# Kernel tuning notes

Hardware: AMD Instinct MI355X
Metric: run time of the kernel (lower is better)

The kernel has to match this reference:

```python
import jax, jax.numpy as jnp
import numpy as np
from itertools import combinations

B, J, D, H, L, DFF = 2048, 7, 128, 8, 4, 512
TH, GH = 4, 4  # triplet cross-attn heads (min(4,128//32)), group-transformer heads

def _build_static():
    trips = list(combinations(range(J), 3))
    tid = {t: i for i, t in enumerate(trips)}
    member = np.zeros((J, len(trips)), dtype=bool)
    for i, t in enumerate(trips):
        for j in t:
            member[j, i] = True
    isr_l, g1_l, g2_l = [], [], []
    for isr in range(J):
        rem = [j for j in range(J) if j != isr]
        for c in combinations(rem, 3):
            comp = tuple(j for j in rem if j not in c)
            if c < comp:
                isr_l.append(isr); g1_l.append(c); g2_l.append(comp)
    return (np.array(trips), member, np.array(isr_l), np.array(g1_l), np.array(g2_l),
            np.array([tid[t] for t in g1_l]), np.array([tid[t] for t in g2_l]))

TRIPS, MEMBER, ISR_IDX, G1_JETS, G2_JETS, G1_TID, G2_TID = _build_static()
N_ASSIGN = len(ISR_IDX)  # 70
TCA_MASK = np.where(MEMBER, 0.0, -1e9).astype(np.float32)  # (J, 35) jet-restricted mask

def _gelu(x):
    return jax.nn.gelu(x, approximate=False)

def _ln(x, g, b, eps=1e-5):
    mu = x.mean(-1, keepdims=True)
    v = ((x - mu) ** 2).mean(-1, keepdims=True)
    return (x - mu) / jnp.sqrt(v + eps) * g + b

def _attend(q, k, v, nhead, bias=None):
    Bq, Lq, d = q.shape
    Lk = k.shape[1]
    dh = d // nhead
    qh = q.reshape(Bq, Lq, nhead, dh)
    kh = k.reshape(Bq, Lk, nhead, dh)
    vh = v.reshape(Bq, Lk, nhead, dh)
    s = jnp.einsum('bqhd,bkhd->bhqk', qh, kh) / np.float32(np.sqrt(dh))
    if bias is not None:
        s = s + bias
    a = jax.nn.softmax(s, -1)
    return jnp.einsum('bhqk,bkhd->bqhd', a, vh).reshape(Bq, Lq, d)

def _enc_layer(x, Wqkv, bqkv, Wo, bo, g1, b1, g2, b2, W1, bb1, W2, bb2, nhead, bias=None):
    # pre-LN TransformerEncoderLayer (norm_first=True, relu activation, eval mode)
    h = _ln(x, g1, b1)
    q, k, v = jnp.split(h @ Wqkv + bqkv, 3, axis=-1)
    x = x + _attend(q, k, v, nhead, bias) @ Wo + bo
    h2 = _ln(x, g2, b2)
    return x + jax.nn.relu(h2 @ W1 + bb1) @ W2 + bb2

def _feat6(p):
    E, px, py, pz = p[..., 0], p[..., 1], p[..., 2], p[..., 3]
    pt = jnp.sqrt(px ** 2 + py ** 2)
    p3 = jnp.sqrt(pt ** 2 + pz ** 2)
    m = jnp.sqrt(jnp.maximum(E ** 2 - p3 ** 2, 1e-8))
    eta = jnp.arcsinh(pz / jnp.maximum(pt, 1e-8))
    phi = jnp.arctan2(py, px)
    return jnp.stack([m, pt, eta, phi, E, p3], -1)

def _forward(four_momenta, W_in, b_in, pt_w, dr_w, mass_w, enc_Wqkv, enc_bqkv, enc_Wo, enc_bo, enc_g1, enc_b1, enc_g2, enc_b2, enc_W1, enc_bb1, enc_W2, enc_bb2, tca_Wq, tca_bq, tca_Wk, tca_bk, tca_Wv, tca_bv, tca_Wo, tca_bo, tca_g1, tca_b1, tca_W1, tca_bb1, tca_W2, tca_bb2, tca_g2, tca_b2, gt_Wqkv, gt_bqkv, gt_Wo, gt_bo, gt_g1, gt_b1, gt_g2, gt_b2, gt_W1, gt_bb1, gt_W2, gt_bb2, ph_g, ph_b, s_W1, s_b1, s_W2, s_b2, s_W3, s_b3):
    fm = four_momenta
    E, px, py, pz = fm[..., 0], fm[..., 1], fm[..., 2], fm[..., 3]
    pt = jnp.maximum(jnp.sqrt(px ** 2 + py ** 2), 1e-8)
    log_pt = jnp.log(pt)
    eta = jnp.arcsinh(pz / pt)
    phi = jnp.arctan2(py, px)
    m_jet = jnp.sqrt(jnp.maximum(E ** 2 - px ** 2 - py ** 2 - pz ** 2, 1e-8))
    x = jnp.concatenate([fm, jnp.stack([log_pt, eta, phi, m_jet], -1)], -1) @ W_in + b_in

    # fused per-head additive attention biases: pT hierarchy, deltaR, pair invariant mass
    pt_b = log_pt[:, :, None] - log_pt[:, None, :]
    cphi, sphi = px / pt, py / pt
    deta = eta[:, :, None] - eta[:, None, :]
    cdphi = jnp.clip(cphi[:, :, None] * cphi[:, None, :] + sphi[:, :, None] * sphi[:, None, :], -1.0 + 1e-7, 1.0 - 1e-7)
    dr_b = jnp.sqrt(deta ** 2 + jnp.arccos(cdphi) ** 2)
    Es = E[:, :, None] + E[:, None, :]
    ps2 = (px[:, :, None] + px[:, None, :]) ** 2 + (py[:, :, None] + py[:, None, :]) ** 2 + (pz[:, :, None] + pz[:, None, :]) ** 2
    mass_b = 0.5 * jnp.log(jnp.maximum(Es ** 2 - ps2, 1e-8))
    bias = (pt_w[None, :, None, None] * pt_b[:, None] + dr_w[None, :, None, None] * dr_b[:, None] + mass_w[None, :, None, None] * mass_b[:, None])  # (B,H,J,J)

    for i in range(L):
        x = _enc_layer(x, enc_Wqkv[i], enc_bqkv[i], enc_Wo[i], enc_bo[i], enc_g1[i], enc_b1[i], enc_g2[i], enc_b2[i], enc_W1[i], enc_bb1[i], enc_W2[i], enc_bb2[i], H, bias)
    jet_emb = x  # (B, J, D)

    # jet-restricted triplet cross-attention over the C(7,3)=35 triplet bank
    triplet_emb = jet_emb[:, TRIPS].mean(2)  # (B, 35, D)
    q = jet_emb @ tca_Wq + tca_bq
    k = triplet_emb @ tca_Wk + tca_bk
    v = triplet_emb @ tca_Wv + tca_bv
    attn = _attend(q, k, v, TH, jnp.asarray(TCA_MASK)[None, None]) @ tca_Wo + tca_bo
    jet_emb = _ln(jet_emb + attn, tca_g1, tca_b1)
    ff = _gelu(jet_emb @ tca_W1 + tca_bb1) @ tca_W2 + tca_bb2
    jet_emb = _ln(jet_emb + ff, tca_g2, tca_b2)

    # GroupTransformer over all unique 3-jet groups in parallel, mean-pool readout
    nT = len(TRIPS)
    gt_in = jet_emb[:, TRIPS].reshape(B * nT, 3, D)
    gt_out = _enc_layer(gt_in, gt_Wqkv, gt_bqkv, gt_Wo, gt_bo, gt_g1, gt_b1, gt_g2, gt_b2, gt_W1, gt_bb1, gt_W2, gt_bb2, GH)
    group_emb = gt_out.mean(1).reshape(B, nT, D)  # (B, 35, D)

    g1e = group_emb[:, G1_TID]  # (B, 70, D)
    g2e = group_emb[:, G2_TID]
    pair_sum = g1e + g2e
    pair_prod = g1e * g2e
    pair_sqdiff = (g1e - g2e) ** 2
    isr_emb = jet_emb[:, ISR_IDX]  # (B, 70, D)
    event_emb = jnp.broadcast_to(jet_emb.mean(1)[:, None], (B, N_ASSIGN, D))

    p_g1 = fm[:, G1_JETS].sum(2)  # (B, 70, 4)
    p_g2 = fm[:, G2_JETS].sum(2)
    p_isr = fm[:, ISR_IDX]
    physics = jnp.concatenate([_feat6(p_g1), _feat6(p_g2), _feat6(p_isr), _feat6(p_g1 + p_g2)], -1)  # (B,70,24)
    physics = _ln(physics, ph_g, ph_b)

    feats = jnp.concatenate([isr_emb, pair_sum, pair_prod, pair_sqdiff, event_emb, physics], -1)  # (B,70,5D+24)
    h = _gelu(feats @ s_W1 + s_b1)
    h = _gelu(h @ s_W2 + s_b2)
    return (h @ s_W3 + s_b3)[..., 0]  # (B, 70) assignment logits


def setup_inputs():
    key = jax.random.key(0)
    ks = iter(jax.random.split(key, 100))
    def nrm(shape, s=0.02):
        return jax.random.normal(next(ks), shape, jnp.float32) * s
    p3 = jax.random.normal(next(ks), (B, J, 3), jnp.float32) * 50.0
    mm = jnp.abs(jax.random.normal(next(ks), (B, J), jnp.float32)) * 20.0 + 5.0
    E = jnp.sqrt((p3 ** 2).sum(-1) + mm ** 2)
    d = {'four_momenta': jnp.concatenate([E[..., None], p3], -1)}
    d.update(W_in=nrm((8, D)), b_in=jnp.zeros((D,)),
             pt_w=nrm((H,), 0.1), dr_w=nrm((H,), 0.1), mass_w=nrm((H,), 0.1),
             enc_Wqkv=nrm((L, D, 3 * D)), enc_bqkv=jnp.zeros((L, 3 * D)),
             enc_Wo=nrm((L, D, D)), enc_bo=jnp.zeros((L, D)),
             enc_g1=jnp.ones((L, D)), enc_b1=jnp.zeros((L, D)),
             enc_g2=jnp.ones((L, D)), enc_b2=jnp.zeros((L, D)),
             enc_W1=nrm((L, D, DFF)), enc_bb1=jnp.zeros((L, DFF)),
             enc_W2=nrm((L, DFF, D)), enc_bb2=jnp.zeros((L, D)),
             tca_Wq=nrm((D, D)), tca_bq=jnp.zeros((D,)),
             tca_Wk=nrm((D, D)), tca_bk=jnp.zeros((D,)),
             tca_Wv=nrm((D, D)), tca_bv=jnp.zeros((D,)),
             tca_Wo=nrm((D, D)), tca_bo=jnp.zeros((D,)),
             tca_g1=jnp.ones((D,)), tca_b1=jnp.zeros((D,)),
             tca_W1=nrm((D, 2 * D)), tca_bb1=jnp.zeros((2 * D,)),
             tca_W2=nrm((2 * D, D)), tca_bb2=jnp.zeros((D,)),
             tca_g2=jnp.ones((D,)), tca_b2=jnp.zeros((D,)),
             gt_Wqkv=nrm((D, 3 * D)), gt_bqkv=jnp.zeros((3 * D,)),
             gt_Wo=nrm((D, D)), gt_bo=jnp.zeros((D,)),
             gt_g1=jnp.ones((D,)), gt_b1=jnp.zeros((D,)),
             gt_g2=jnp.ones((D,)), gt_b2=jnp.zeros((D,)),
             gt_W1=nrm((D, 2 * D)), gt_bb1=jnp.zeros((2 * D,)),
             gt_W2=nrm((2 * D, D)), gt_bb2=jnp.zeros((D,)),
             ph_g=jnp.ones((24,)), ph_b=jnp.zeros((24,)),
             s_W1=nrm((5 * D + 24, 2 * D)), s_b1=jnp.zeros((2 * D,)),
             s_W2=nrm((2 * D, D)), s_b2=jnp.zeros((D,)),
             s_W3=nrm((D, 1)), s_b3=jnp.zeros((1,)))
    return d


def reference(four_momenta, W_in, b_in, pt_w, dr_w, mass_w, enc_Wqkv, enc_bqkv, enc_Wo, enc_bo, enc_g1, enc_b1, enc_g2, enc_b2, enc_W1, enc_bb1, enc_W2, enc_bb2, tca_Wq, tca_bq, tca_Wk, tca_bk, tca_Wv, tca_bv, tca_Wo, tca_bo, tca_g1, tca_b1, tca_W1, tca_bb1, tca_W2, tca_bb2, tca_g2, tca_b2, gt_Wqkv, gt_bqkv, gt_Wo, gt_bo, gt_g1, gt_b1, gt_g2, gt_b2, gt_W1, gt_bb1, gt_W2, gt_bb2, ph_g, ph_b, s_W1, s_b1, s_W2, s_b2, s_W3, s_b3):
    return _forward(four_momenta, W_in, b_in, pt_w, dr_w, mass_w, enc_Wqkv, enc_bqkv, enc_Wo, enc_bo, enc_g1, enc_b1, enc_g2, enc_b2, enc_W1, enc_bb1, enc_W2, enc_bb2, tca_Wq, tca_bq, tca_Wk, tca_bk, tca_Wv, tca_bv, tca_Wo, tca_bo, tca_g1, tca_b1, tca_W1, tca_bb1, tca_W2, tca_bb2, tca_g2, tca_b2, gt_Wqkv, gt_bqkv, gt_Wo, gt_bo, gt_g1, gt_b1, gt_g2, gt_b2, gt_W1, gt_bb1, gt_W2, gt_bb2, ph_g, ph_b, s_W1, s_b1, s_W2, s_b2, s_W3, s_b3)
```

## Files before the change

### kernel.cpp

```cpp
#include <hip/hip_runtime.h>
#include <hip/hip_bf16.h>
#include <math.h>

typedef __hip_bfloat16 bf16;

constexpr int NB=2048, NJ=7, ND=128, NHD=8, NLYR=4, NFF=512, NTR=35, NAS=70;
constexpr int SD=132, S256=260, S384=388, S512=516;

struct KArgs { const void* p[54]; void* out; const void* flag; };

__device__ __forceinline__ float bfbits(unsigned short s){ return __uint_as_float(((unsigned)s)<<16); }
__device__ __forceinline__ float ldv(const float* p, size_t i){ return p[i]; }
__device__ __forceinline__ float ldv(const bf16* p, size_t i){ return __bfloat162float(p[i]); }
__device__ __forceinline__ void ldv4(const float* p, size_t i, float* o){
  const float4 v=*reinterpret_cast<const float4*>(p+i);
  o[0]=v.x; o[1]=v.y; o[2]=v.z; o[3]=v.w;
}
__device__ __forceinline__ void ldv4(const bf16* p, size_t i, float* o){
  unsigned long long u=*reinterpret_cast<const unsigned long long*>((const unsigned short*)p+i);
  o[0]=bfbits((unsigned short)u);
  o[1]=bfbits((unsigned short)(u>>16));
  o[2]=bfbits((unsigned short)(u>>32));
  o[3]=bfbits((unsigned short)(u>>48));
}
__device__ __forceinline__ void stv(float* p, size_t i, float v){ p[i]=v; }
__device__ __forceinline__ void stv(bf16* p, size_t i, float v){ p[i]=__float2bfloat16(v); }
__device__ __forceinline__ float gelu_f(float x){ return 0.5f*x*(1.0f+erff(x*0.70710678118654752f)); }

__device__ void build_trips(int* tr){
  int n=0;
  for(int a=0;a<NJ;a++)for(int b=a+1;b<NJ;b++)for(int c=b+1;c<NJ;c++){
    tr[n*3+0]=a; tr[n*3+1]=b; tr[n*3+2]=c; n++;
  }
}
__device__ int find_tid(const int* tr,int a,int b,int c){
  for(int t=0;t<NTR;t++) if(tr[t*3]==a&&tr[t*3+1]==b&&tr[t*3+2]==c) return t;
  return 0;
}
__device__ void build_assign(const int* tr,int* isr,int* g1t,int* g2t,int* g1j,int* g2j){
  int n=0;
  for(int is=0;is<NJ;is++){
    int rem[6],m=0;
    for(int j=0;j<NJ;j++) if(j!=is) rem[m++]=j;
    for(int i=0;i<6;i++)for(int jj=i+1;jj<6;jj++)for(int k=jj+1;k<6;k++){
      int c0=rem[i],c1=rem[jj],c2=rem[k];
      int comp[3],q=0;
      for(int r=0;r<6;r++){ int v=rem[r]; if(v!=c0&&v!=c1&&v!=c2) comp[q++]=v; }
      bool lt=(c0<comp[0])||(c0==comp[0]&&(c1<comp[1]||(c1==comp[1]&&c2<comp[2])));
      if(lt){
        isr[n]=is;
        g1j[n*3]=c0; g1j[n*3+1]=c1; g1j[n*3+2]=c2;
        g2j[n*3]=comp[0]; g2j[n*3+1]=comp[1]; g2j[n*3+2]=comp[2];
        g1t[n]=find_tid(tr,c0,c1,c2);
        g2t[n]=find_tid(tr,comp[0],comp[1],comp[2]);
        n++;
      }
    }
  }
}

template<typename T>
__device__ void lnr(const float* src, int ASs, float* dst, int ASd, const T* g, const T* bb,
                    float* mu, float* rs, int rows, int tid, int NT){
  for(int r0=0;r0<rows;r0+=(NT>>5)){
    int row=r0+(tid>>5), lane=tid&31;
    if(row<rows){
      const float* s=src+row*ASs;
      float m=0.f,v=0.f;
      for(int d=lane;d<ND;d+=32){ float t=s[d]; m+=t; v+=t*t; }
      for(int off=16;off>0;off>>=1){ m+=__shfl_down(m,off,32); v+=__shfl_down(v,off,32); }
      if(lane==0){ m*=(1.f/ND); float vv=v*(1.f/ND)-m*m; mu[row]=m; rs[row]=rsqrtf(fmaxf(vv,0.f)+1e-5f); }
    }
    __syncthreads();
  }
  for(int idx=tid; idx<rows*ND; idx+=NT){
    int j=idx>>7, d=idx&127;
    dst[j*ASd+d]=(src[j*ASs+d]-mu[j])*rs[j]*ldv(g,d)+ldv(bb,d);
  }
  __syncthreads();
}

template<typename T>
__device__ void mm4b(const float* a, int ASa, const T* W, const T* bias, float* out, int ASo,
                     int M, int K, int N, int tid, int NT, int act, bool accum, int RB){
  int NQ=N>>2;
  int CGS=NT/RB;
  if(tid<CGS*RB){
    int i=tid%RB, cg0=tid/RB;
    if(i<M){
      const float* ar=a+i*ASa;
      for(int cg=cg0; cg<NQ; cg+=CGS){
        int k4=cg<<2;
        float acc[4];
        if(bias) ldv4(bias,k4,acc);
        else { acc[0]=0.f;acc[1]=0.f;acc[2]=0.f;acc[3]=0.f; }
        for(int d=0; d<K; d++){
          float w[4]; ldv4(W,(size_t)d*N+k4,w);
          float av=ar[d];
          acc[0]+=av*w[0]; acc[1]+=av*w[1]; acc[2]+=av*w[2]; acc[3]+=av*w[3];
        }
        int o=i*ASo+k4;
        #pragma unroll
        for(int j=0;j<4;j++){
          float v=acc[j];
          if(act==1) v=fmaxf(v,0.f); else if(act==2) v=gelu_f(v);
          if(accum) out[o+j]+=v; else out[o+j]=v;
        }
      }
    }
  }
  __syncthreads();
}

__global__ void k_detect(const unsigned short* w, int n, unsigned* flag){
  __shared__ int bad[256];
  int tid=threadIdx.x;
  int my=0;
  for(int i=tid;i<n;i+=256){
    unsigned e=(w[i]>>7)&0xFFu;
    if(e>=134u) my=1;
  }
  bad[tid]=my;
  __syncthreads();
  if(tid==0){
    int any=0; for(int i=0;i<256;i++) any|=bad[i];
    flag[0]= any?1u:0u;
  }
}


template<typename T>
__device__ void phase_embed(const T* fm, const T* Win, const T* bin,
                            const T* ptw, const T* drw, const T* mw,
                            float* xS, float* biasS, float* scratch, int b, int tid, int NT){
  float* fE =scratch+0;  float* fpx=scratch+8;  float* fpy=scratch+16; float* fpz=scratch+24;
  float* flp=scratch+32; float* fet=scratch+40; float* fcp=scratch+48; float* fsp=scratch+56;
  float* fph=scratch+64; float* fms=scratch+72;
  if(tid<NJ){
    size_t base=((size_t)b*NJ+tid)*4;
    float e=ldv(fm,base+0), x_=ldv(fm,base+1), y_=ldv(fm,base+2), z_=ldv(fm,base+3);
    float pt=fmaxf(sqrtf(x_*x_+y_*y_),1e-8f);
    fE[tid]=e; fpx[tid]=x_; fpy[tid]=y_; fpz[tid]=z_;
    flp[tid]=logf(pt);
    fet[tid]=asinhf(z_/pt);
    fph[tid]=atan2f(y_,x_);
    fms[tid]=sqrtf(fmaxf(e*e-x_*x_-y_*y_-z_*z_,1e-8f));
    fcp[tid]=x_/pt; fsp[tid]=y_/pt;
  }
  __syncthreads();
  for(int idx=tid; idx<NJ*ND; idx+=NT){
    int j=idx>>7, d=idx&127;
    float in8[8]={fE[j],fpx[j],fpy[j],fpz[j],flp[j],fet[j],fph[j],fms[j]};
    float acc=ldv(bin,d);
    for(int c=0;c<8;c++) acc += in8[c]*ldv(Win,c*ND+d);
    xS[j*SD+d]=acc;
  }
  for(int idx=tid; idx<NHD*NJ*NJ; idx+=NT){
    int h=idx/49, r=idx%49, i=r/7, jj=r%7;
    float ptb=flp[i]-flp[jj];
    float deta=fet[i]-fet[jj];
    float cd=fcp[i]*fcp[jj]+fsp[i]*fsp[jj];
    cd=fminf(fmaxf(cd,-1.0f+1e-7f),1.0f-1e-7f);
    float ac=acosf(cd);
    float dr=sqrtf(deta*deta+ac*ac);
    float Es=fE[i]+fE[jj];
    float sx=fpx[i]+fpx[jj], sy=fpy[i]+fpy[jj], sz=fpz[i]+fpz[jj];
    float mb=0.5f*logf(fmaxf(Es*Es-(sx*sx+sy*sy+sz*sz),1e-8f));
    biasS[idx]=ldv(ptw,h)*ptb+ldv(drw,h)*dr+ldv(mw,h)*mb;
  }
  __syncthreads();
}

template<typename T>
__device__ void phase_enc(float* xS, const float* biasS, float* P, float* muS, float* rsS,
    const T* eWqkv,const T* ebqkv,const T* eWo,const T* ebo,
    const T* eg1,const T* eb1,const T* eg2,const T* eb2,
    const T* eW1,const T* ebb1,const T* eW2,const T* ebb2, int tid, int NT){
  float* h  =P+0;
  float* qkv=P+924;
  float* att=P+3640;
  float* sb =P+4564;
  float* ff =P+924;
  for(int l=0;l<NLYR;l++){
    lnr(xS,SD,h,SD,eg1+l*ND,eb1+l*ND,muS,rsS,NJ,tid,NT);
    mm4b(h,SD,eWqkv+(size_t)l*ND*3*ND,ebqkv+l*3*ND,qkv,S384,NJ,ND,3*ND,tid,NT,0,false,8);
    for(int idx=tid;idx<NHD*NJ*NJ;idx+=NT){
      int hh=idx/49, r=idx%49, i=r/7, jj=r%7;
      float acc=0.f;
      const float* qr=&qkv[i*S384+hh*16];
      const float* kr=&qkv[jj*S384+128+hh*16];
      for(int d=0;d<16;d++) acc+=qr[d]*kr[d];
      sb[idx]=acc*0.25f+biasS[idx];
    }
    __syncthreads();
    if(tid<NHD*NJ){
      float* s=&sb[tid*7];
      float mx=s[0]; for(int j=1;j<7;j++) mx=fmaxf(mx,s[j]);
      float sm=0.f; for(int j=0;j<7;j++){ s[j]=expf(s[j]-mx); sm+=s[j]; }
      float inv=1.0f/sm; for(int j=0;j<7;j++) s[j]*=inv;
    }
    __syncthreads();
    for(int idx=tid;idx<NJ*ND;idx+=NT){
      int i=idx>>7, d=idx&127, hh=d>>4;
      float acc=0.f;
      for(int j=0;j<7;j++) acc+=sb[(hh*7+i)*7+j]*qkv[j*S384+256+d];
      att[i*SD+d]=acc;
    }
    __syncthreads();
    mm4b(att,SD,eWo+(size_t)l*ND*ND,ebo+l*ND,xS,SD,NJ,ND,ND,tid,NT,0,true,8);
    lnr(xS,SD,h,SD,eg2+l*ND,eb2+l*ND,muS,rsS,NJ,tid,NT);
    mm4b(h,SD,eW1+(size_t)l*ND*NFF,ebb1+l*NFF,ff,S512,NJ,ND,NFF,tid,NT,1,false,8);
    mm4b(ff,S512,eW2+(size_t)l*NFF*ND,ebb2+l*ND,xS,SD,NJ,NFF,ND,tid,NT,0,true,8);
  }
}

template<typename T>
__device__ void trip_proj(const float* xS, const int* trS, const T* W, const T* bias,
                          float* out, int tid, int NT){
  int CGS=NT>>3;
  for(int base=0;base<NTR;base+=8){
    int t=base+(tid&7);
    if(t<NTR){
      int a0=trS[t*3]*SD, a1=trS[t*3+1]*SD, a2=trS[t*3+2]*SD;
      for(int cg=tid>>3; cg<32; cg+=CGS){
        int k4=cg<<2;
        float acc[4]; ldv4(bias,k4,acc);
        for(int c=0;c<ND;c++){
          float tv=(xS[a0+c]+xS[a1+c]+xS[a2+c])*(1.0f/3.0f);
          float w[4]; ldv4(W,(size_t)c*ND+k4,w);
          acc[0]+=tv*w[0]; acc[1]+=tv*w[1]; acc[2]+=tv*w[2]; acc[3]+=tv*w[3];
        }
        int o=t*SD+k4;
        out[o]=acc[0]; out[o+1]=acc[1]; out[o+2]=acc[2]; out[o+3]=acc[3];
      }
    }
  }
  __syncthreads();
}

template<typename T>
__device__ void phase_tca(float* xS, float* P, float* muS, float* rsS, const int* trS,
    const T* tWq,const T* tbq,const T* tWk,const T* tbk,const T* tWv,const T* tbv,
    const T* tWo,const T* tbo,const T* tg1,const T* tb1,const T* tW1,const T* tbb1,
    const T* tW2,const T* tbb2,const T* tg2,const T* tb2, int tid, int NT){
  float* q   =P+0;
  float* kv  =P+924;
  float* sb4 =P+5544;
  float* att2=P+6524;
  float* tff =P+0;
  const float sc=0.17677669529663687f;
  mm4b(xS,SD,tWq,tbq,q,SD,NJ,ND,ND,tid,NT,0,false,8);
  trip_proj(xS,trS,tWk,tbk,kv,tid,NT);
  for(int idx=tid;idx<4*NJ*NTR;idx+=NT){
    int hh=idx/245, r=idx%245, i=r/35, t=r%35;
    float acc=0.f;
    const float* qr=&q[i*SD+hh*32];
    const float* kr=&kv[t*SD+hh*32];
    for(int d=0;d<32;d++) acc+=qr[d]*kr[d];
    bool mem=(trS[t*3]==i||trS[t*3+1]==i||trS[t*3+2]==i);
    sb4[idx]=acc*sc+(mem?0.0f:-1e9f);
  }
  __syncthreads();
  if(tid<4*NJ){
    float* s=&sb4[tid*35];
    float mx=-3e38f; for(int t=0;t<35;t++) mx=fmaxf(mx,s[t]);
    float sm=0.f; for(int t=0;t<35;t++){ s[t]=expf(s[t]-mx); sm+=s[t]; }
    float inv=1.0f/sm; for(int t=0;t<35;t++) s[t]*=inv;
  }
  __syncthreads();
  trip_proj(xS,trS,tWv,tbv,kv,tid,NT);
  for(int idx=tid;idx<NJ*ND;idx+=NT){
    int i=idx>>7, d=idx&127, hh=d>>5;
    float acc=0.f;
    for(int t=0;t<35;t++) acc+=sb4[(hh*7+i)*35+t]*kv[t*SD+d];
    att2[i*SD+d]=acc;
  }
  __syncthreads();
  mm4b(att2,SD,tWo,tbo,xS,SD,NJ,ND,ND,tid,NT,0,true,8);
  lnr(xS,SD,xS,SD,tg1,tb1,muS,rsS,NJ,tid,NT);
  mm4b(xS,SD,tW1,tbb1,tff,S256,NJ,ND,2*ND,tid,NT,2,false,8);
  mm4b(tff,S256,tW2,tbb2,xS,SD,NJ,2*ND,ND,tid,NT,0,true,8);
  lnr(xS,SD,xS,SD,tg2,tb2,muS,rsS,NJ,tid,NT);
}


template<typename T>
__global__ __launch_bounds__(256) void k_front(KArgs A, unsigned want, float* X2, float* EVT){
  if(((const unsigned*)A.flag)[0]!=want) return;
  int b=blockIdx.x, tid=threadIdx.x;
  __shared__ float xS[NJ*SD];
  __shared__ float biasS[NHD*NJ*NJ];
  __shared__ float P[7448];
  __shared__ float muS[16], rsS[16];
  __shared__ int trS[NTR*3];
  if(tid==0) build_trips(trS);
  __syncthreads();
  phase_embed((const T*)A.p[0],(const T*)A.p[1],(const T*)A.p[2],
              (const T*)A.p[3],(const T*)A.p[4],(const T*)A.p[5],xS,biasS,P,b,tid,256);
  phase_enc(xS,biasS,P,muS,rsS,
    (const T*)A.p[6],(const T*)A.p[7],(const T*)A.p[8],(const T*)A.p[9],
    (const T*)A.p[10],(const T*)A.p[11],(const T*)A.p[12],(const T*)A.p[13],
    (const T*)A.p[14],(const T*)A.p[15],(const T*)A.p[16],(const T*)A.p[17],tid,256);
  phase_tca(xS,P,muS,rsS,trS,
    (const T*)A.p[18],(const T*)A.p[19],(const T*)A.p[20],(const T*)A.p[21],
    (const T*)A.p[22],(const T*)A.p[23],(const T*)A.p[24],(const T*)A.p[25],
    (const T*)A.p[26],(const T*)A.p[27],(const T*)A.p[28],(const T*)A.p[29],
    (const T*)A.p[30],(const T*)A.p[31],(const T*)A.p[32],(const T*)A.p[33],tid,256);
  for(int idx=tid;idx<NJ*ND;idx+=256) X2[(size_t)b*NJ*ND+idx]=xS[(idx>>7)*SD+(idx&127)];
  if(tid<ND){
    float s=0.f; for(int j=0;j<NJ;j++) s+=xS[j*SD+tid];
    EVT[(size_t)b*ND+tid]=s*(1.0f/NJ);
  }
}

template<typename T>
__global__ __launch_bounds__(512,8) void k_gt(KArgs A, unsigned want, const float* X2, float* GRP){
  if(((const unsigned*)A.flag)[0]!=want) return;
  const T* gWqkv=(const T*)A.p[34]; const T* gbqkv=(const T*)A.p[35];
  const T* gWo  =(const T*)A.p[36]; const T* gbo  =(const T*)A.p[37];
  const T* gg1  =(const T*)A.p[38]; const T* gb1  =(const T*)A.p[39];
  const T* gg2  =(const T*)A.p[40]; const T* gb2  =(const T*)A.p[41];
  const T* gW1  =(const T*)A.p[42]; const T* gbb1 =(const T*)A.p[43];
  const T* gW2  =(const T*)A.p[44]; const T* gbb2 =(const T*)A.p[45];
  int b=blockIdx.x/12, ch=blockIdx.x%12, tid=threadIdx.x;
  int c0=ch*3, tc=(NTR-c0)<3?(NTR-c0):3;
  int ntok=3*tc;
  __shared__ float jets[NJ*SD];
  __shared__ float xg[9*SD];
  __shared__ float hg[9*SD];
  __shared__ float qkvg[9*S384];
  __shared__ float sbg[108];
  __shared__ float muS[16], rsS[16];
  __shared__ int trS[NTR*3];
  if(tid==0) build_trips(trS);
  for(int idx=tid;idx<NJ*ND;idx+=512) jets[(idx>>7)*SD+(idx&127)]=X2[(size_t)b*NJ*ND+idx];
  __syncthreads();
  const float sc=0.17677669529663687f;
  for(int idx=tid;idx<ntok*ND;idx+=512){
    int s=idx>>7, d=idx&127; int t=c0+s/3, r=s%3;
    xg[s*SD+d]=jets[trS[t*3+r]*SD+d];
  }
  __syncthreads();
  lnr(xg,SD,hg,SD,gg1,gb1,muS,rsS,ntok,tid,512);
  mm4b(hg,SD,gWqkv,gbqkv,qkvg,S384,ntok,ND,3*ND,tid,512,0,false,9);
  for(int idx=tid;idx<tc*36;idx+=512){
    int s=idx/36, r=idx%36, hh=r/9, p=r%9, i=p/3, j=p%3;
    float acc=0.f;
    const float* qr=&qkvg[(s*3+i)*S384+hh*32];
    const float* kr=&qkvg[(s*3+j)*S384+128+hh*32];
    for(int d=0;d<32;d++) acc+=qr[d]*kr[d];
    sbg[idx]=acc*sc;
  }
  __syncthreads();
  for(int q2=tid;q2<tc*12;q2+=512){
    int s=q2/12, r2=q2%12;
    float* base=&sbg[s*36+(r2/3)*9+(r2%3)*3];
    float mx=fmaxf(base[0],fmaxf(base[1],base[2]));
    float e0=expf(base[0]-mx),e1=expf(base[1]-mx),e2=expf(base[2]-mx);
    float inv=1.0f/(e0+e1+e2);
    base[0]=e0*inv; base[1]=e1*inv; base[2]=e2*inv;
  }
  __syncthreads();
  for(int idx=tid;idx<ntok*ND;idx+=512){
    int sr=idx>>7, d=idx&127; int s=sr/3, i=sr%3, hh=d>>5;
    float acc=0.f;
    for(int j=0;j<3;j++) acc+=sbg[s*36+hh*9+i*3+j]*qkvg[(s*3+j)*S384+256+d];
    hg[sr*SD+d]=acc;
  }
  __syncthreads();
  mm4b(hg,SD,gWo,gbo,xg,SD,ntok,ND,ND,tid,512,0,true,9);
  lnr(xg,SD,hg,SD,gg2,gb2,muS,rsS,ntok,tid,512);
  mm4b(hg,SD,gW1,gbb1,qkvg,S256,ntok,ND,2*ND,tid,512,1,false,9);
  mm4b(qkvg,S256,gW2,gbb2,xg,SD,ntok,2*ND,ND,tid,512,0,true,9);
  for(int idx=tid;idx<tc*ND;idx+=512){
    int s=idx>>7, d=idx&127;
    GRP[((size_t)b*NTR+c0+s)*ND+d]=
      (xg[(s*3)*SD+d]+xg[(s*3+1)*SD+d]+xg[(s*3+2)*SD+d])*(1.0f/3.0f);
  }
}

template<typename T>
__global__ __launch_bounds__(512) void k_score(KArgs A, unsigned want,
    const float* X2, const float* EVT, const float* GRP){
  if(((const unsigned*)A.flag)[0]!=want) return;
  const T* fm =(const T*)A.p[0];
  const T* phg=(const T*)A.p[46]; const T* phb=(const T*)A.p[47];
  const T* sW1=(const T*)A.p[48]; const T* sb1=(const T*)A.p[49];
  const T* sW2=(const T*)A.p[50]; const T* sb2=(const T*)A.p[51];
  const T* sW3=(const T*)A.p[52]; const T* sb3=(const T*)A.p[53];
  T* OUT=(T*)A.out;
  int b=blockIdx.x, tid=threadIdx.x;
  int ar=tid&7, cg=tid>>3;

  __shared__ float POOL[12472];
  float* grpP=POOL;
  float* Ws  =POOL+4680;
  float* h2t =POOL+4680;
  float* h1c =POOL+8776;
  float* Fc  =POOL+10096;
  float* jets=POOL+10096;
  __shared__ float physAll[72*24];
  __shared__ float isrc[7*260];
  __shared__ float evtc[256];
  __shared__ float evtS[128];
  __shared__ float fmvS[28];
  __shared__ int trS[105];
  __shared__ int isrS[72], g1tS[72], g2tS[72], g1jS[216], g2jS[216];

  if(tid==0){
    build_trips(trS); build_assign(trS,isrS,g1tS,g2tS,g1jS,g2jS);
    for(int a=70;a<72;a++){
      isrS[a]=0; g1tS[a]=0; g2tS[a]=0;
      for(int r=0;r<3;r++){ g1jS[a*3+r]=0; g2jS[a*3+r]=0; }
    }
  }
  for(int idx=tid;idx<NTR*ND;idx+=512) grpP[(idx>>7)*132+(idx&127)]=GRP[(size_t)b*NTR*ND+idx];
  for(int idx=tid;idx<NJ*ND;idx+=512) jets[idx]=X2[(size_t)b*NJ*ND+idx];
  if(tid<ND) evtS[tid]=EVT[(size_t)b*ND+tid];
  if(tid>=128&&tid<128+NJ*4){ int q=tid-128; fmvS[q]=ldv(fm,(size_t)b*NJ*4+q); }
  __syncthreads();

  {
    int i=tid&7, k4=(tid>>3)<<2;
    const float* src=(i<7)?(jets+i*ND):evtS;
    size_t rb=(i<7)?0:(size_t)4*ND;
    float acc[4];
    if(i==7) ldv4(sb1,k4,acc); else { acc[0]=0.f;acc[1]=0.f;acc[2]=0.f;acc[3]=0.f; }
    for(int d=0;d<ND;d++){
      float w[4]; ldv4(sW1,(rb+d)*2*ND+k4,w);
      float av=src[d];
      acc[0]+=av*w[0]; acc[1]+=av*w[1]; acc[2]+=av*w[2]; acc[3]+=av*w[3];
    }
    if(i<7){ int o=i*260+k4; isrc[o]=acc[0]; isrc[o+1]=acc[1]; isrc[o+2]=acc[2]; isrc[o+3]=acc[3]; }
    else   { evtc[k4]=acc[0]; evtc[k4+1]=acc[1]; evtc[k4+2]=acc[2]; evtc[k4+3]=acc[3]; }
  }
  if(tid<72*4){
    int a=tid>>2, g=tid&3;
    float* o=&physAll[a*24+g*6];
    if(a<NAS){
      float p[4];
      #pragma unroll
      for(int c=0;c<4;c++){
        float v;
        if(g==0)      v=fmvS[g1jS[a*3]*4+c]+fmvS[g1jS[a*3+1]*4+c]+fmvS[g1jS[a*3+2]*4+c];
        else if(g==1) v=fmvS[g2jS[a*3]*4+c]+fmvS[g2jS[a*3+1]*4+c]+fmvS[g2jS[a*3+2]*4+c];
        else if(g==2) v=fmvS[isrS[a]*4+c];
        else          v=fmvS[g1jS[a*3]*4+c]+fmvS[g1jS[a*3+1]*4+c]+fmvS[g1jS[a*3+2]*4+c]
                       +fmvS[g2jS[a*3]*4+c]+fmvS[g2jS[a*3+1]*4+c]+fmvS[g2jS[a*3+2]*4+c];
        p[c]=v;
      }
      float E=p[0], x_=p[1], y_=p[2], z_=p[3];
      float pt=sqrtf(x_*x_+y_*y_);
      float p3=sqrtf(pt*pt+z_*z_);
      float m =sqrtf(fmaxf(E*E-p3*p3,1e-8f));
      float eta=asinhf(z_/fmaxf(pt,1e-8f));
      float ph=atan2f(y_,x_);
      o[0]=m; o[1]=pt; o[2]=eta; o[3]=ph; o[4]=E; o[5]=p3;
    } else { o[0]=0;o[1]=0;o[2]=0;o[3]=0;o[4]=0;o[5]=0; }
  }
  __syncthreads();
  if(tid<72){
    float* o=&physAll[tid*24];
    float m=0.f; for(int c=0;c<24;c++) m+=o[c]; m*=(1.0f/24.0f);
    float v=0.f; for(int c=0;c<24;c++){ float t=o[c]-m; v+=t*t; } v*=(1.0f/24.0f);
    float r=rsqrtf(v+1e-5f);
    for(int c=0;c<24;c++) o[c]=(o[c]-m)*r*ldv(phg,c)+ldv(phb,c);
  }
  __syncthreads();

  for(int t=0;t<2;t++){
    int tbase=t*40;
    int ns=(t==0)?5:4;
    float acc[5][4];
    #pragma unroll
    for(int s=0;s<5;s++){ acc[s][0]=0.f;acc[s][1]=0.f;acc[s][2]=0.f;acc[s][3]=0.f; }

    for(int kc=0;kc<408;kc+=16){
      int csz=(408-kc)<16?(408-kc):16;
      for(int idx4=tid*4; idx4<csz*256; idx4+=2048){
        int d=idx4>>8, n=idx4&255;
        int c=kc+d;
        size_t r=(c<384)? (size_t)(ND+c) : (size_t)(5*ND+(c-384));
        float w[4]; ldv4(sW1,r*2*ND+n,w);
        Ws[d*256+n]=w[0]; Ws[d*256+n+1]=w[1]; Ws[d*256+n+2]=w[2]; Ws[d*256+n+3]=w[3];
      }
      for(int idx=tid; idx<72*16; idx+=512){
        int a=idx>>4, d=idx&15;
        if(d<csz){
          int c=kc+d;
          float f;
          if(c<384){
            int cc=c&127, kind=c>>7;
            float u=grpP[g1tS[a]*132+cc], w=grpP[g2tS[a]*132+cc];
            f=(kind==0)?(u+w):(kind==1)?(u*w):(u-w)*(u-w);
          } else f=physAll[a*24+(c-384)];
          Fc[a*17+d]=f;
        }
      }
      __syncthreads();
      for(int d=0;d<csz;d++){
        const float* wp=&Ws[d*256+(cg<<2)];
        float w0=wp[0],w1=wp[1],w2=wp[2],w3=wp[3];
        #pragma unroll
        for(int s=0;s<5;s++){
          if(s<ns){
            float f=Fc[(tbase+ar+8*s)*17+d];
            acc[s][0]+=f*w0; acc[s][1]+=f*w1; acc[s][2]+=f*w2; acc[s][3]+=f*w3;
          }
        }
      }
      __syncthreads();
    }
    float h1r[5][4];
    #pragma unroll
    for(int s=0;s<5;s++){
      if(s<ns){
        int a=tbase+ar+8*s;
        int ir=isrS[a];
        #pragma unroll
        for(int j=0;j<4;j++){
          int k=(cg<<2)+j;
          h1r[s][j]=gelu_f(acc[s][j]+evtc[k]+isrc[ir*260+k]);
        }
      } else { h1r[s][0]=0;h1r[s][1]=0;h1r[s][2]=0;h1r[s][3]=0; }
    }

    float acc2[5][4];
    {
      float b2v[4]; int k4b=(cg&31)<<2; ldv4(sb2,k4b,b2v);
      #pragma unroll
      for(int s=0;s<5;s++){ acc2[s][0]=b2v[0];acc2[s][1]=b2v[1];acc2[s][2]=b2v[2];acc2[s][3]=b2v[3]; }
    }
    for(int fc=0;fc<256;fc+=32){
      if(cg>=(fc>>2)&&cg<(fc>>2)+8){
        int dcol=(cg<<2)-fc;
        #pragma unroll
        for(int s=0;s<5;s++){
          if(s<ns){
            int al=ar+8*s;
            h1c[al*33+dcol]  =h1r[s][0];
            h1c[al*33+dcol+1]=h1r[s][1];
            h1c[al*33+dcol+2]=h1r[s][2];
            h1c[al*33+dcol+3]=h1r[s][3];
          }
        }
      }
      for(int idx4=tid*4; idx4<32*128; idx4+=2048){
        int d=idx4>>7, n=idx4&127;
        float w[4]; ldv4(sW2,(size_t)(fc+d)*128+n,w);
        Ws[d*128+n]=w[0]; Ws[d*128+n+1]=w[1]; Ws[d*128+n+2]=w[2]; Ws[d*128+n+3]=w[3];
      }
      __syncthreads();
      if(cg<32){
        for(int d=0;d<32;d++){
          const float* wp=&Ws[d*128+(cg<<2)];
          float w0=wp[0],w1=wp[1],w2=wp[2],w3=wp[3];
          #pragma unroll
          for(int s=0;s<5;s++){
            if(s<ns){
              float f=h1c[(ar+8*s)*33+d];
              acc2[s][0]+=f*w0; acc2[s][1]+=f*w1; acc2[s][2]+=f*w2; acc2[s][3]+=f*w3;
            }
          }
        }
      }
      __syncthreads();
    }
    if(cg<32){
      int k4=cg<<2;
      #pragma unroll
      for(int s=0;s<5;s++){
        if(s<ns){
          int al=ar+8*s;
          h2t[al*129+k4]  =gelu_f(acc2[s][0]);
          h2t[al*129+k4+1]=gelu_f(acc2[s][1]);
          h2t[al*129+k4+2]=gelu_f(acc2[s][2]);
          h2t[al*129+k4+3]=gelu_f(acc2[s][3]);
        }
      }
    }
    __syncthreads();
    {
      int widx=tid>>6, lane=tid&63;
      int nal=(t==0)?40:30;
      for(int s2=0;s2<5;s2++){
        int al=widx+8*s2;
        if(al<nal){
          float part=h2t[al*129+lane]*ldv(sW3,lane)+h2t[al*129+64+lane]*ldv(sW3,64+lane);
          for(int off=32;off>0;off>>=1) part+=__shfl_down(part,off,64);
          if(lane==0) stv(OUT,(size_t)b*NAS+tbase+al,part+ldv(sb3,0));
        }
      }
    }
    __syncthreads();
  }
}

extern "C" void kernel_launch(void* const* d_in, const int* in_sizes, int n_in,
                              void* d_out, int out_size, void* d_ws, size_t ws_size,
                              hipStream_t stream){
  KArgs A;
  for(int i=0;i<54;i++) A.p[i]=d_in[i];
  A.out=d_out;
  A.flag=d_ws;

  float* ws=(float*)d_ws;
  float* X2  = ws+16;
  float* EVT = X2 + (size_t)NB*NJ*ND;
  float* GRP = EVT + (size_t)NB*ND;

  k_detect<<<1,256,0,stream>>>((const unsigned short*)d_in[1],1024,(unsigned*)d_ws);

  k_front<bf16> <<<NB,256,0,stream>>>(A,0u,X2,EVT);
  k_front<float><<<NB,256,0,stream>>>(A,1u,X2,EVT);
  k_gt<bf16>    <<<NB*12,512,0,stream>>>(A,0u,X2,GRP);
  k_gt<float>   <<<NB*12,512,0,stream>>>(A,1u,X2,GRP);
  k_score<bf16> <<<NB,512,0,stream>>>(A,0u,X2,EVT,GRP);
  k_score<float><<<NB,512,0,stream>>>(A,1u,X2,EVT,GRP);
}
```

Before: 7.632 ms.

## Replace row-per-thread matmul with column-per-thread register-blocked rows

Replaces the mm4b routine (each thread owning one row and four columns) with a templated mmR in which each thread owns one output column and keeps accumulators for every row in registers. Each weight element is therefore read once per block instead of once per row, cutting global/L2 weight traffic. The triplet K/V projections now precompute the averaged triplet inputs into shared memory once and reuse mmR in row groups of seven. The changes enlarge shared scratch and relax k_gt launch bounds to 6 waves per SIMD to make room for the extra registers, at the cost of fewer threads active when N is smaller than the block size and lower occupancy.

```diff
diff --git a/kernel.cpp b/kernel.cpp
--- a/kernel.cpp
+++ b/kernel.cpp
@@ -80,33 +80,26 @@
   __syncthreads();
 }
 
-template<typename T>
-__device__ void mm4b(const float* a, int ASa, const T* W, const T* bias, float* out, int ASo,
-                     int M, int K, int N, int tid, int NT, int act, bool accum, int RB){
-  int NQ=N>>2;
-  int CGS=NT/RB;
-  if(tid<CGS*RB){
-    int i=tid%RB, cg0=tid/RB;
-    if(i<M){
-      const float* ar=a+i*ASa;
-      for(int cg=cg0; cg<NQ; cg+=CGS){
-        int k4=cg<<2;
-        float acc[4];
-        if(bias) ldv4(bias,k4,acc);
-        else { acc[0]=0.f;acc[1]=0.f;acc[2]=0.f;acc[3]=0.f; }
-        for(int d=0; d<K; d++){
-          float w[4]; ldv4(W,(size_t)d*N+k4,w);
-          float av=ar[d];
-          acc[0]+=av*w[0]; acc[1]+=av*w[1]; acc[2]+=av*w[2]; acc[3]+=av*w[3];
-        }
-        int o=i*ASo+k4;
-        #pragma unroll
-        for(int j=0;j<4;j++){
-          float v=acc[j];
-          if(act==1) v=fmaxf(v,0.f); else if(act==2) v=gelu_f(v);
-          if(accum) out[o+j]+=v; else out[o+j]=v;
-        }
-      }
+template<int K,int N,int RMAX,typename T>
+__device__ void mmR(const float* a,int ASa,const T* W,const T* bias,float* out,int ASo,
+                    int M,int tid,int NT,int act,bool accum){
+  for(int col=tid; col<N; col+=NT){
+    float acc[RMAX];
+    #pragma unroll
+    for(int r=0;r<RMAX;r++) acc[r]=0.f;
+    #pragma unroll 4
+    for(int d=0;d<K;d++){
+      float w=ldv(W,(size_t)d*N+col);
+      #pragma unroll
+      for(int r=0;r<RMAX;r++) if(r<M) acc[r]+=a[r*ASa+d]*w;
+    }
+    float bv = bias? ldv(bias,col) : 0.f;
+    #pragma unroll
+    for(int r=0;r<RMAX;r++) if(r<M){
+      float v=acc[r]+bv;
+      if(act==1) v=fmaxf(v,0.f); else if(act==2) v=gelu_f(v);
+      int o=r*ASo+col;
+      if(accum) out[o]+=v; else out[o]=v;
     }
   }
   __syncthreads();
@@ -183,7 +176,7 @@
   float* ff =P+924;
   for(int l=0;l<NLYR;l++){
     lnr(xS,SD,h,SD,eg1+l*ND,eb1+l*ND,muS,rsS,NJ,tid,NT);
-    mm4b(h,SD,eWqkv+(size_t)l*ND*3*ND,ebqkv+l*3*ND,qkv,S384,NJ,ND,3*ND,tid,NT,0,false,8);
+    mmR<128,384,7>(h,SD,eWqkv+(size_t)l*ND*3*ND,ebqkv+l*3*ND,qkv,S384,NJ,tid,NT,0,false);
     for(int idx=tid;idx<NHD*NJ*NJ;idx+=NT){
       int hh=idx/49, r=idx%49, i=r/7, jj=r%7;
       float acc=0.f;
@@ -207,35 +200,11 @@
       att[i*SD+d]=acc;
     }
     __syncthreads();
-    mm4b(att,SD,eWo+(size_t)l*ND*ND,ebo+l*ND,xS,SD,NJ,ND,ND,tid,NT,0,true,8);
+    mmR<128,128,7>(att,SD,eWo+(size_t)l*ND*ND,ebo+l*ND,xS,SD,NJ,tid,NT,0,true);
     lnr(xS,SD,h,SD,eg2+l*ND,eb2+l*ND,muS,rsS,NJ,tid,NT);
-    mm4b(h,SD,eW1+(size_t)l*ND*NFF,ebb1+l*NFF,ff,S512,NJ,ND,NFF,tid,NT,1,false,8);
-    mm4b(ff,S512,eW2+(size_t)l*NFF*ND,ebb2+l*ND,xS,SD,NJ,NFF,ND,tid,NT,0,true,8);
-  }
-}
-
-template<typename T>
-__device__ void trip_proj(const float* xS, const int* trS, const T* W, const T* bias,
-                          float* out, int tid, int NT){
-  int CGS=NT>>3;
-  for(int base=0;base<NTR;base+=8){
-    int t=base+(tid&7);
-    if(t<NTR){
-      int a0=trS[t*3]*SD, a1=trS[t*3+1]*SD, a2=trS[t*3+2]*SD;
-      for(int cg=tid>>3; cg<32; cg+=CGS){
-        int k4=cg<<2;
-        float acc[4]; ldv4(bias,k4,acc);
-        for(int c=0;c<ND;c++){
-          float tv=(xS[a0+c]+xS[a1+c]+xS[a2+c])*(1.0f/3.0f);
-          float w[4]; ldv4(W,(size_t)c*ND+k4,w);
-          acc[0]+=tv*w[0]; acc[1]+=tv*w[1]; acc[2]+=tv*w[2]; acc[3]+=tv*w[3];
-        }
-        int o=t*SD+k4;
-        out[o]=acc[0]; out[o+1]=acc[1]; out[o+2]=acc[2]; out[o+3]=acc[3];
-      }
-    }
-  }
-  __syncthreads();
+    mmR<128,512,7>(h,SD,eW1+(size_t)l*ND*NFF,ebb1+l*NFF,ff,S512,NJ,tid,NT,1,false);
+    mmR<512,128,7>(ff,S512,eW2+(size_t)l*NFF*ND,ebb2+l*ND,xS,SD,NJ,tid,NT,0,true);
+  }
 }
 
 template<typename T>
@@ -243,14 +212,21 @@
     const T* tWq,const T* tbq,const T* tWk,const T* tbk,const T* tWv,const T* tbv,
     const T* tWo,const T* tbo,const T* tg1,const T* tb1,const T* tW1,const T* tbb1,
     const T* tW2,const T* tbb2,const T* tg2,const T* tb2, int tid, int NT){
-  float* q   =P+0;
-  float* kv  =P+924;
-  float* sb4 =P+5544;
-  float* att2=P+6524;
+  float* A   =P+0;
+  float* kv  =P+4620;
+  float* q   =P+9240;
+  float* sb4 =P+10164;
+  float* att2=P+0;
   float* tff =P+0;
   const float sc=0.17677669529663687f;
-  mm4b(xS,SD,tWq,tbq,q,SD,NJ,ND,ND,tid,NT,0,false,8);
-  trip_proj(xS,trS,tWk,tbk,kv,tid,NT);
+  for(int idx=tid;idx<NTR*ND;idx+=NT){
+    int t=idx>>7, d=idx&127;
+    A[t*SD+d]=(xS[trS[t*3]*SD+d]+xS[trS[t*3+1]*SD+d]+xS[trS[t*3+2]*SD+d])*(1.0f/3.0f);
+  }
+  __syncthreads();
+  mmR<128,128,7>(xS,SD,tWq,tbq,q,SD,NJ,tid,NT,0,false);
+  for(int rg=0;rg<5;rg++)
+    mmR<128,128,7>(A+rg*7*SD,SD,tWk,tbk,kv+rg*7*SD,SD,7,tid,NT,0,false);
   for(int idx=tid;idx<4*NJ*NTR;idx+=NT){
     int hh=idx/245, r=idx%245, i=r/35, t=r%35;
     float acc=0.f;
@@ -268,7 +244,8 @@
     float inv=1.0f/sm; for(int t=0;t<35;t++) s[t]*=inv;
   }
   __syncthreads();
-  trip_proj(xS,trS,tWv,tbv,kv,tid,NT);
+  for(int rg=0;rg<5;rg++)
+    mmR<128,128,7>(A+rg*7*SD,SD,tWv,tbv,kv+rg*7*SD,SD,7,tid,NT,0,false);
   for(int idx=tid;idx<NJ*ND;idx+=NT){
     int i=idx>>7, d=idx&127, hh=d>>5;
     float acc=0.f;
@@ -276,10 +253,10 @@
     att2[i*SD+d]=acc;
   }
   __syncthreads();
-  mm4b(att2,SD,tWo,tbo,xS,SD,NJ,ND,ND,tid,NT,0,true,8);
+  mmR<128,128,7>(att2,SD,tWo,tbo,xS,SD,NJ,tid,NT,0,true);
   lnr(xS,SD,xS,SD,tg1,tb1,muS,rsS,NJ,tid,NT);
-  mm4b(xS,SD,tW1,tbb1,tff,S256,NJ,ND,2*ND,tid,NT,2,false,8);
-  mm4b(tff,S256,tW2,tbb2,xS,SD,NJ,2*ND,ND,tid,NT,0,true,8);
+  mmR<128,256,7>(xS,SD,tW1,tbb1,tff,S256,NJ,tid,NT,2,false);
+  mmR<256,128,7>(tff,S256,tW2,tbb2,xS,SD,NJ,tid,NT,0,true);
   lnr(xS,SD,xS,SD,tg2,tb2,muS,rsS,NJ,tid,NT);
 }
 
@@ -290,7 +267,7 @@
   int b=blockIdx.x, tid=threadIdx.x;
   __shared__ float xS[NJ*SD];
   __shared__ float biasS[NHD*NJ*NJ];
-  __shared__ float P[7448];
+  __shared__ float P[11200];
   __shared__ float muS[16], rsS[16];
   __shared__ int trS[NTR*3];
   if(tid==0) build_trips(trS);
@@ -314,7 +291,7 @@
 }
 
 template<typename T>
-__global__ __launch_bounds__(512,8) void k_gt(KArgs A, unsigned want, const float* X2, float* GRP){
+__global__ __launch_bounds__(512,6) void k_gt(KArgs A, unsigned want, const float* X2, float* GRP){
   if(((const unsigned*)A.flag)[0]!=want) return;
   const T* gWqkv=(const T*)A.p[34]; const T* gbqkv=(const T*)A.p[35];
   const T* gWo  =(const T*)A.p[36]; const T* gbo  =(const T*)A.p[37];
@@ -342,7 +319,7 @@
   }
   __syncthreads();
   lnr(xg,SD,hg,SD,gg1,gb1,muS,rsS,ntok,tid,512);
-  mm4b(hg,SD,gWqkv,gbqkv,qkvg,S384,ntok,ND,3*ND,tid,512,0,false,9);
+  mmR<128,384,9>(hg,SD,gWqkv,gbqkv,qkvg,S384,ntok,tid,512,0,false);
   for(int idx=tid;idx<tc*36;idx+=512){
     int s=idx/36, r=idx%36, hh=r/9, p=r%9, i=p/3, j=p%3;
     float acc=0.f;
@@ -368,10 +345,10 @@
     hg[sr*SD+d]=acc;
   }
   __syncthreads();
-  mm4b(hg,SD,gWo,gbo,xg,SD,ntok,ND,ND,tid,512,0,true,9);
+  mmR<128,128,9>(hg,SD,gWo,gbo,xg,SD,ntok,tid,512,0,true);
   lnr(xg,SD,hg,SD,gg2,gb2,muS,rsS,ntok,tid,512);
-  mm4b(hg,SD,gW1,gbb1,qkvg,S256,ntok,ND,2*ND,tid,512,1,false,9);
-  mm4b(qkvg,S256,gW2,gbb2,xg,SD,ntok,2*ND,ND,tid,512,0,true,9);
+  mmR<128,256,9>(hg,SD,gW1,gbb1,qkvg,S256,ntok,tid,512,1,false);
+  mmR<256,128,9>(qkvg,S256,gW2,gbb2,xg,SD,ntok,tid,512,0,true);
   for(int idx=tid;idx<tc*ND;idx+=512){
     int s=idx>>7, d=idx&127;
     GRP[((size_t)b*NTR+c0+s)*ND+d]=
```

New measurement: 6.968 ms. 1.1x faster.
